# Kernel tuning notes

Measured on AMD Instinct MI355X. Metric: run time of the kernel, lower is better.

The kernel has to match this reference:

```python
import jax, jax.numpy as jnp
import numpy as np

E = 1024          # n_embed_dim
H = 64            # head_size = n_embed_dim // n_heads (16)

def setup_inputs() -> dict:
    key = jax.random.key(0)
    k_x, k_q, k_k, k_v = jax.random.split(key, 4)
    scale = 1.0 / np.sqrt(E)
    return {
        "x": jax.random.normal(k_x, (4, 2048, E), dtype=jnp.float32),
        "ln_gamma": jnp.ones((E,), jnp.float32),
        "ln_beta": jnp.zeros((E,), jnp.float32),
        # torch nn.Linear weights: [out_features, in_features]
        "Wq": jax.random.normal(k_q, (H, E), dtype=jnp.float32) * scale,
        "Wk": jax.random.normal(k_k, (H, E), dtype=jnp.float32) * scale,
        "Wv": jax.random.normal(k_v, (H, E), dtype=jnp.float32) * scale,
    }

def reference(x, ln_gamma, ln_beta, Wq, Wk, Wv):
    # LayerNorm over last dim (eps matches torch default 1e-5)
    mu = jnp.mean(x, axis=-1, keepdims=True)
    var = jnp.mean(jnp.square(x - mu), axis=-1, keepdims=True)
    xn = (x - mu) * jax.lax.rsqrt(var + 1e-5) * ln_gamma + ln_beta

    q = jnp.einsum('bse,he->bsh', xn, Wq)   # [B,S,H]
    k = jnp.einsum('bse,he->bsh', xn, Wk)
    v = jnp.einsum('bse,he->bsh', xn, Wv)

    scores = jnp.einsum('bqh,bkh->bqk', q, k) / jnp.sqrt(jnp.float32(H))
    S = x.shape[1]
    causal = jnp.tril(jnp.ones((S, S), dtype=bool))
    scores = jnp.where(causal, scores, -jnp.inf)
    attn = jax.nn.softmax(scores, axis=-1)
    return jnp.einsum('bqk,bkh->bqh', attn, v)
```

## Files before the change

kernel.cpp:

```cpp
#include <hip/hip_runtime.h>

#define E 1024
#define HH 64
#define BB 4
#define SS 2048
#define BS (BB*SS)
#define NSLOT 144

typedef unsigned short u16;
typedef short bf16x8 __attribute__((ext_vector_type(8)));
typedef float f32x4 __attribute__((ext_vector_type(4)));

#define LOG2E_O8 0.18033688011112042f

__device__ inline u16 f2bf(float f) {
    unsigned int u = __float_as_uint(f);
    unsigned int r = (u + 0x7FFFu + ((u >> 16) & 1u)) >> 16;
    return (u16)r;
}
__device__ inline float bf2f(u16 h) {
    return __uint_as_float(((unsigned int)h) << 16);
}

__global__ __launch_bounds__(256) void ln_wcast(const float* __restrict__ x,
        const float* __restrict__ gamma, const float* __restrict__ beta,
        const float* __restrict__ Wq, const float* __restrict__ Wk,
        const float* __restrict__ Wv,
        u16* __restrict__ xn, u16* __restrict__ wc) {
    const int t = threadIdx.x;
    if (blockIdx.x < 2048) {
        const int w = t >> 6, lane = t & 63;
        const size_t row = (size_t)blockIdx.x * 4 + w;
        const float4* xr = (const float4*)(x + row * E);
        float4 v[4];
        #pragma unroll
        for (int i = 0; i < 4; ++i) v[i] = xr[lane + 64 * i];
        float s = 0.f, sq = 0.f;
        #pragma unroll
        for (int i = 0; i < 4; ++i) {
            s  += v[i].x + v[i].y + v[i].z + v[i].w;
            sq += v[i].x*v[i].x + v[i].y*v[i].y + v[i].z*v[i].z + v[i].w*v[i].w;
        }
        #pragma unroll
        for (int off = 32; off > 0; off >>= 1) {
            s  += __shfl_xor(s,  off);
            sq += __shfl_xor(sq, off);
        }
        const float mean = s * (1.0f / E);
        const float var  = sq * (1.0f / E) - mean * mean;
        const float rstd = rsqrtf(var + 1e-5f);
        const float4* gr = (const float4*)gamma;
        const float4* br = (const float4*)beta;
        #pragma unroll
        for (int i = 0; i < 4; ++i) {
            const float4 g  = gr[lane + 64 * i];
            const float4 bt = br[lane + 64 * i];
            ushort4 o;
            o.x = f2bf((v[i].x - mean) * rstd * g.x + bt.x);
            o.y = f2bf((v[i].y - mean) * rstd * g.y + bt.y);
            o.z = f2bf((v[i].z - mean) * rstd * g.z + bt.z);
            o.w = f2bf((v[i].w - mean) * rstd * g.w + bt.w);
            *(ushort4*)(xn + row * E + (lane + 64 * i) * 4) = o;
        }
    } else {
        const int row = blockIdx.x - 2048;
        const float* src = (row < 64)  ? (Wq + (size_t)row * E)
                         : (row < 128) ? (Wk + (size_t)(row - 64) * E)
                                       : (Wv + (size_t)(row - 128) * E);
        const float sc = (row < 64) ? LOG2E_O8 : 1.0f;
        const float4 v = *(const float4*)(src + t * 4);
        ushort4 o;
        o.x = f2bf(v.x * sc); o.y = f2bf(v.y * sc);
        o.z = f2bf(v.z * sc); o.w = f2bf(v.w * sc);
        *(ushort4*)(wc + (size_t)row * E + t * 4) = o;
    }
}

__global__ __launch_bounds__(256) void qkv_mfma(const u16* __restrict__ xn,
        const u16* __restrict__ wc,
        u16* __restrict__ qb, u16* __restrict__ kb, u16* __restrict__ vt) {
    const int mb   = blockIdx.x >> 1;
    const int half = blockIdx.x & 1;
    const int row0 = mb * 32;
    const int t = threadIdx.x;
    const int w = t >> 6, lane = t & 63;
    const int quad = lane >> 4, r15 = lane & 15;
    const int mt = w >> 1, cgrp = w & 1;
    __shared__ u16 Xs[32 * 128];
    __shared__ u16 Ws[96 * 128];
    f32x4 acc[3] = {};
    const int xrow = mt * 16 + r15;

    for (int kc8 = 0; kc8 < 8; ++kc8) {
        __syncthreads();
        {
            const int row = t >> 3, ch = t & 7;
            #pragma unroll
            for (int hf = 0; hf < 2; ++hf) {
                const uint4 d = *(const uint4*)(xn + (size_t)(row0 + row) * E
                                                + kc8 * 128 + hf * 64 + ch * 8);
                *(uint4*)&Xs[row * 128 + hf * 64 + (ch ^ (row & 7)) * 8] = d;
            }
        }
        #pragma unroll
        for (int i = 0; i < 6; ++i) {
            const int idx = i * 256 + t;
            const int wl = idx >> 4, ch16 = idx & 15;
            const int hf = ch16 >> 3, ch = ch16 & 7;
            const uint4 d = *(const uint4*)(wc + (size_t)(half * 96 + wl) * E
                                            + kc8 * 128 + hf * 64 + ch * 8);
            *(uint4*)&Ws[wl * 128 + hf * 64 + (ch ^ (wl & 7)) * 8] = d;
        }
        __syncthreads();
        #pragma unroll
        for (int kk = 0; kk < 4; ++kk) {
            const int hf = kk >> 1, q4 = (kk & 1) * 4 + quad;
            const bf16x8 af = *(const bf16x8*)&Xs[xrow * 128 + hf * 64 + (q4 ^ (xrow & 7)) * 8];
            #pragma unroll
            for (int j = 0; j < 3; ++j) {
                const int wl = (cgrp * 3 + j) * 16 + r15;
                const bf16x8 bfr = *(const bf16x8*)&Ws[wl * 128 + hf * 64 + (q4 ^ (wl & 7)) * 8];
                acc[j] = __builtin_amdgcn_mfma_f32_16x16x32_bf16(af, bfr, acc[j], 0, 0, 0);
            }
        }
    }
    const int b    = row0 >> 11;
    const int key0 = row0 & 2047;
    #pragma unroll
    for (int j = 0; j < 3; ++j) {
        const int cg  = half * 96 + cgrp * 48 + j * 16 + r15;
        const int sel = cg >> 6;
        const int col = cg & 63;
        if (sel < 2) {
            u16* base = (sel == 0) ? qb : kb;
            #pragma unroll
            for (int r = 0; r < 4; ++r) {
                const size_t row = (size_t)row0 + mt * 16 + quad * 4 + r;
                base[row * HH + col] = f2bf(acc[j][r]);
            }
        } else {
            ushort4 pk;
            pk.x = f2bf(acc[j][0]); pk.y = f2bf(acc[j][1]);
            pk.z = f2bf(acc[j][2]); pk.w = f2bf(acc[j][3]);
            *(ushort4*)(vt + (size_t)b * HH * SS + (size_t)col * SS
                           + key0 + mt * 16 + quad * 4) = pk;
        }
    }
}

__global__ __launch_bounds__(256) void attn_partial(const u16* __restrict__ qb,
        const u16* __restrict__ kb, const u16* __restrict__ vt,
        u16* __restrict__ po, float* __restrict__ pl,
        float* __restrict__ out) {
    const int bid = blockIdx.x;
    const int b   = bid / 72;
    const int s2  = bid - b * 72;
    int a = (int)((sqrtf(4.0f * s2 + 1.0f) - 1.0f) * 0.5f);
    while ((a + 1) * (a + 2) <= s2) ++a;
    while (a * (a + 1) > s2) --a;
    const int rem = s2 - a * (a + 1);
    const int rp  = rem / (a + 1);
    const int c   = rem - rp * (a + 1);
    const int qt0 = 4 * a + 2 * rp;
    const int nc  = a + 1;
    const int t = threadIdx.x;
    const int w = t >> 6, lane = t & 63;
    const int quad = lane >> 4, r15 = lane & 15;

    __shared__ u16 Ks[4 * 64 * 64];
    __shared__ u16 VT[4 * 64 * 64];
    __shared__ u16 Ps[64 * 64];

    bf16x8 qf0[2], qf1[2];
    #pragma unroll
    for (int qi = 0; qi < 2; ++qi) {
        const size_t qrow = ((size_t)b * SS + (qt0 + qi) * 64 + w * 16 + r15) * HH;
        qf0[qi] = *(const bf16x8*)(qb + qrow + quad * 8);
        qf1[qi] = *(const bf16x8*)(qb + qrow + 32 + quad * 8);
    }

    const int ntmax = (c < a) ? 4 : (2 * rp + 2);

    {
        const int row = t >> 2, ch0 = (t & 3) * 2;
        for (int tl = 0; tl < ntmax; ++tl) {
            const int kt = (c * 4 + tl) << 6;
            const uint4* srcK = (const uint4*)(kb + ((size_t)b * SS + kt + row) * HH + ch0 * 8);
            const uint4 k0 = srcK[0], k1 = srcK[1];
            *(uint4*)&Ks[tl * 4096 + row * 64 + ((ch0    ) ^ (row & 7)) * 8] = k0;
            *(uint4*)&Ks[tl * 4096 + row * 64 + ((ch0 + 1) ^ (row & 7)) * 8] = k1;
            const uint4* srcV = (const uint4*)(vt + (size_t)b * HH * SS + (size_t)row * SS
                                               + kt + ch0 * 8);
            const uint4 v0 = srcV[0], v1 = srcV[1];
            *(uint4*)&VT[tl * 4096 + row * 64 + ((ch0    ) ^ (row & 7)) * 8] = v0;
            *(uint4*)&VT[tl * 4096 + row * 64 + ((ch0 + 1) ^ (row & 7)) * 8] = v1;
        }
    }
    __syncthreads();

    f32x4 o[2][4] = {};
    float l_[2][4] = {};

    for (int tl = 0; tl < ntmax; ++tl) {
        const int tile = c * 4 + tl;
        const u16* KsT = &Ks[tl * 4096];
        const u16* VTT = &VT[tl * 4096];

        bf16x8 kf0[4], kf1[4], vf0[4], vf1[4];
        #pragma unroll
        for (int nt = 0; nt < 4; ++nt) {
            const int krow = nt * 16 + r15;
            kf0[nt] = *(const bf16x8*)&KsT[krow * 64 + ((    quad) ^ (krow & 7)) * 8];
            kf1[nt] = *(const bf16x8*)&KsT[krow * 64 + ((4 + quad) ^ (krow & 7)) * 8];
            vf0[nt] = *(const bf16x8*)&VTT[krow * 64 + ((    quad) ^ (krow & 7)) * 8];
            vf1[nt] = *(const bf16x8*)&VTT[krow * 64 + ((4 + quad) ^ (krow & 7)) * 8];
        }

        #pragma unroll
        for (int qi = 0; qi < 2; ++qi) {
            const int qt_i = qt0 + qi;
            if (tile > qt_i) continue;

            f32x4 s4[4] = {};
            #pragma unroll
            for (int nt = 0; nt < 4; ++nt) {
                s4[nt] = __builtin_amdgcn_mfma_f32_16x16x32_bf16(qf0[qi], kf0[nt], s4[nt], 0, 0, 0);
                s4[nt] = __builtin_amdgcn_mfma_f32_16x16x32_bf16(qf1[qi], kf1[nt], s4[nt], 0, 0, 0);
            }
            if (tile == qt_i) {
                #pragma unroll
                for (int nt = 0; nt < 4; ++nt)
                    #pragma unroll
                    for (int r = 0; r < 4; ++r)
                        if (nt * 16 + r15 > w * 16 + quad * 4 + r) s4[nt][r] = -INFINITY;
            }

            float p[4][4];
            #pragma unroll
            for (int r = 0; r < 4; ++r) {
                #pragma unroll
                for (int nt = 0; nt < 4; ++nt)
                    p[nt][r] = __builtin_amdgcn_exp2f(s4[nt][r]);
                l_[qi][r] += (p[0][r] + p[1][r]) + (p[2][r] + p[3][r]);
            }

            #pragma unroll
            for (int nt = 0; nt < 4; ++nt)
                #pragma unroll
                for (int r = 0; r < 4; ++r) {
                    const int prow = w * 16 + quad * 4 + r;
                    const int col  = nt * 16 + r15;
                    Ps[prow * 64 + (((col >> 3) ^ (prow & 7)) * 8) + (col & 7)] = f2bf(p[nt][r]);
                }
            const int arow = w * 16 + r15;
            const bf16x8 pf0 = *(const bf16x8*)&Ps[arow * 64 + ((    quad) ^ (arow & 7)) * 8];
            const bf16x8 pf1 = *(const bf16x8*)&Ps[arow * 64 + ((4 + quad) ^ (arow & 7)) * 8];

            #pragma unroll
            for (int ht = 0; ht < 4; ++ht) {
                o[qi][ht] = __builtin_amdgcn_mfma_f32_16x16x32_bf16(pf0, vf0[ht], o[qi][ht], 0, 0, 0);
                o[qi][ht] = __builtin_amdgcn_mfma_f32_16x16x32_bf16(pf1, vf1[ht], o[qi][ht], 0, 0, 0);
            }
        }
    }

    #pragma unroll
    for (int qi = 0; qi < 2; ++qi)
        #pragma unroll
        for (int r = 0; r < 4; ++r) {
            l_[qi][r] += __shfl_xor(l_[qi][r], 1); l_[qi][r] += __shfl_xor(l_[qi][r], 2);
            l_[qi][r] += __shfl_xor(l_[qi][r], 4); l_[qi][r] += __shfl_xor(l_[qi][r], 8);
        }

    #pragma unroll
    for (int qi = 0; qi < 2; ++qi) {
        const int qt_i = qt0 + qi;
        if (nc == 1) {
            #pragma unroll
            for (int r = 0; r < 4; ++r) {
                const float inv = 1.0f / l_[qi][r];
                const size_t orow = ((size_t)b * SS + qt_i * 64 + w * 16 + quad * 4 + r) * HH;
                #pragma unroll
                for (int ht = 0; ht < 4; ++ht)
                    out[orow + ht * 16 + r15] = o[qi][ht][r] * inv;
            }
        } else {
            const int slot = b * NSLOT + 2 * a * (a + 1) + (2 * rp + qi) * (a + 1) + c;
            #pragma unroll
            for (int r = 0; r < 4; ++r) {
                const int q = w * 16 + quad * 4 + r;
                #pragma unroll
                for (int ht = 0; ht < 4; ++ht)
                    po[(size_t)slot * 4096 + q * 64 + ht * 16 + r15] = f2bf(o[qi][ht][r]);
                if (r15 == 0) pl[slot * 64 + q] = l_[qi][r];
            }
        }
    }
}

__global__ __launch_bounds__(256) void attn_reduce(const u16* __restrict__ po,
        const float* __restrict__ pl, float* __restrict__ out) {
    const int bid = blockIdx.x;
    const int b = bid / 112, rem = bid - b * 112;
    const int qt = 4 + (rem >> 2), qq = rem & 3;
    const int a = qt >> 2, r_ = qt & 3;
    const int nc = a + 1;
    const int sbase = b * NSLOT + 2 * a * (a + 1) + r_ * (a + 1);
    const int t = threadIdx.x;
    const int h = t & 63, qr = t >> 6;
    #pragma unroll
    for (int i = 0; i < 4; ++i) {
        const int q = qq * 16 + qr * 4 + i;
        float osum = 0.f, lsum = 0.f;
        for (int cidx = 0; cidx < nc; ++cidx) {
            osum += bf2f(po[(size_t)(sbase + cidx) * 4096 + q * 64 + h]);
            lsum += pl[(sbase + cidx) * 64 + q];
        }
        out[((size_t)b * SS + (qt << 6) + q) * HH + h] = osum / lsum;
    }
}

extern "C" void kernel_launch(void* const* d_in, const int* in_sizes, int n_in,
                              void* d_out, int out_size, void* d_ws, size_t ws_size,
                              hipStream_t stream) {
    const float* x     = (const float*)d_in[0];
    const float* gamma = (const float*)d_in[1];
    const float* beta  = (const float*)d_in[2];
    const float* Wq    = (const float*)d_in[3];
    const float* Wk    = (const float*)d_in[4];
    const float* Wv    = (const float*)d_in[5];
    float* out = (float*)d_out;

    char* p = (char*)d_ws;
    u16*   xn   = (u16*)p;                         p += (size_t)BS * E * 2;
    u16*   wc   = (u16*)p;                         p += 393216;
    u16*   qb   = (u16*)p;                         p += (size_t)BS * HH * 2;
    u16*   kb   = (u16*)p;                         p += (size_t)BS * HH * 2;
    u16*   vt   = (u16*)p;                         p += (size_t)BS * HH * 2;
    u16*   po   = (u16*)p;                         p += (size_t)BB * NSLOT * 4096 * 2;
    float* pl   = (float*)p;

    ln_wcast    <<<2048 + 192,  256, 0, stream>>>(x, gamma, beta, Wq, Wk, Wv, xn, wc);
    qkv_mfma    <<<BS / 16,     256, 0, stream>>>(xn, wc, qb, kb, vt);
    attn_partial<<<BB * 72,     256, 0, stream>>>(qb, kb, vt, po, pl, out);
    attn_reduce <<<BB * 112,    256, 0, stream>>>(po, pl, out);
}
```

Baseline: 118.8 us.

## Fuse attention split-K reduce into partial kernel via atomic last-block counter

Removes the separate attn_reduce launch. Each partial block now increments a per-(batch, query-tile-pair) atomic counter, and the last-arriving block sums the bf16 partial outputs and row sums and writes the final output. The counters are zeroed by an extra block in the layernorm kernel. This saves one kernel launch and its tail, but the final reduction is serialized onto a single block per group, and it adds threadfence and atomic overhead.

Result: slower. 200.4 us (+68.7%).

```diff
diff --git a/kernel.cpp b/kernel.cpp
--- a/kernel.cpp
+++ b/kernel.cpp
@@ -26,7 +26,7 @@
         const float* __restrict__ gamma, const float* __restrict__ beta,
         const float* __restrict__ Wq, const float* __restrict__ Wk,
         const float* __restrict__ Wv,
-        u16* __restrict__ xn, u16* __restrict__ wc) {
+        u16* __restrict__ xn, u16* __restrict__ wc, int* __restrict__ cnt) {
     const int t = threadIdx.x;
     if (blockIdx.x < 2048) {
         const int w = t >> 6, lane = t & 63;
@@ -62,6 +62,8 @@
             o.w = f2bf((v[i].w - mean) * rstd * g.w + bt.w);
             *(ushort4*)(xn + row * E + (lane + 64 * i) * 4) = o;
         }
+    } else if (blockIdx.x == 2240) {
+        if (t < 64) cnt[t] = 0;
     } else {
         const int row = blockIdx.x - 2048;
         const float* src = (row < 64)  ? (Wq + (size_t)row * E)
@@ -151,7 +153,7 @@
 __global__ __launch_bounds__(256) void attn_partial(const u16* __restrict__ qb,
         const u16* __restrict__ kb, const u16* __restrict__ vt,
         u16* __restrict__ po, float* __restrict__ pl,
-        float* __restrict__ out) {
+        int* __restrict__ cnt, float* __restrict__ out) {
     const int bid = blockIdx.x;
     const int b   = bid / 72;
     const int s2  = bid - b * 72;
@@ -272,10 +274,10 @@
             l_[qi][r] += __shfl_xor(l_[qi][r], 4); l_[qi][r] += __shfl_xor(l_[qi][r], 8);
         }
 
-    #pragma unroll
-    for (int qi = 0; qi < 2; ++qi) {
-        const int qt_i = qt0 + qi;
-        if (nc == 1) {
+    if (nc == 1) {
+        #pragma unroll
+        for (int qi = 0; qi < 2; ++qi) {
+            const int qt_i = qt0 + qi;
             #pragma unroll
             for (int r = 0; r < 4; ++r) {
                 const float inv = 1.0f / l_[qi][r];
@@ -284,39 +286,47 @@
                 for (int ht = 0; ht < 4; ++ht)
                     out[orow + ht * 16 + r15] = o[qi][ht][r] * inv;
             }
-        } else {
-            const int slot = b * NSLOT + 2 * a * (a + 1) + (2 * rp + qi) * (a + 1) + c;
-            #pragma unroll
-            for (int r = 0; r < 4; ++r) {
-                const int q = w * 16 + quad * 4 + r;
-                #pragma unroll
-                for (int ht = 0; ht < 4; ++ht)
-                    po[(size_t)slot * 4096 + q * 64 + ht * 16 + r15] = f2bf(o[qi][ht][r]);
-                if (r15 == 0) pl[slot * 64 + q] = l_[qi][r];
-            }
-        }
-    }
-}
-
-__global__ __launch_bounds__(256) void attn_reduce(const u16* __restrict__ po,
-        const float* __restrict__ pl, float* __restrict__ out) {
-    const int bid = blockIdx.x;
-    const int b = bid / 112, rem = bid - b * 112;
-    const int qt = 4 + (rem >> 2), qq = rem & 3;
-    const int a = qt >> 2, r_ = qt & 3;
-    const int nc = a + 1;
-    const int sbase = b * NSLOT + 2 * a * (a + 1) + r_ * (a + 1);
-    const int t = threadIdx.x;
-    const int h = t & 63, qr = t >> 6;
+        }
+        return;
+    }
+
     #pragma unroll
-    for (int i = 0; i < 4; ++i) {
-        const int q = qq * 16 + qr * 4 + i;
-        float osum = 0.f, lsum = 0.f;
-        for (int cidx = 0; cidx < nc; ++cidx) {
-            osum += bf2f(po[(size_t)(sbase + cidx) * 4096 + q * 64 + h]);
-            lsum += pl[(sbase + cidx) * 64 + q];
-        }
-        out[((size_t)b * SS + (qt << 6) + q) * HH + h] = osum / lsum;
+    for (int qi = 0; qi < 2; ++qi) {
+        const int slot = b * NSLOT + 2 * a * (a + 1) + (2 * rp + qi) * (a + 1) + c;
+        #pragma unroll
+        for (int r = 0; r < 4; ++r) {
+            const int q = w * 16 + quad * 4 + r;
+            #pragma unroll
+            for (int ht = 0; ht < 4; ++ht)
+                po[(size_t)slot * 4096 + q * 64 + ht * 16 + r15] = f2bf(o[qi][ht][r]);
+            if (r15 == 0) pl[slot * 64 + q] = l_[qi][r];
+        }
+    }
+
+    __shared__ int tick;
+    __syncthreads();
+    if (t == 0) {
+        __threadfence();
+        tick = atomicAdd(&cnt[b * 16 + a * 2 + rp], 1);
+    }
+    __syncthreads();
+    if (tick == nc - 1) {
+        __threadfence();
+        const int h = t & 63, qr = t >> 6;
+        #pragma unroll
+        for (int qi = 0; qi < 2; ++qi) {
+            const int qt_i = qt0 + qi;
+            const int sbase = b * NSLOT + 2 * a * (a + 1) + (2 * rp + qi) * (a + 1);
+            for (int i = 0; i < 16; ++i) {
+                const int q = qr * 16 + i;
+                float osum = 0.f, lsum = 0.f;
+                for (int cidx = 0; cidx < nc; ++cidx) {
+                    osum += bf2f(po[(size_t)(sbase + cidx) * 4096 + q * 64 + h]);
+                    lsum += pl[(sbase + cidx) * 64 + q];
+                }
+                out[((size_t)b * SS + (qt_i << 6) + q) * HH + h] = osum / lsum;
+            }
+        }
     }
 }
 
@@ -338,10 +348,10 @@
     u16*   kb   = (u16*)p;                         p += (size_t)BS * HH * 2;
     u16*   vt   = (u16*)p;                         p += (size_t)BS * HH * 2;
     u16*   po   = (u16*)p;                         p += (size_t)BB * NSLOT * 4096 * 2;
-    float* pl   = (float*)p;
-
-    ln_wcast    <<<2048 + 192,  256, 0, stream>>>(x, gamma, beta, Wq, Wk, Wv, xn, wc);
-    qkv_mfma    <<<BS / 16,     256, 0, stream>>>(xn, wc, qb, kb, vt);
-    attn_partial<<<BB * 72,     256, 0, stream>>>(qb, kb, vt, po, pl, out);
-    attn_reduce <<<BB * 112,    256, 0, stream>>>(po, pl, out);
-}
+    float* pl   = (float*)p;                       p += (size_t)BB * NSLOT * 64 * 4;
+    int*   cnt  = (int*)p;
+
+    ln_wcast    <<<2048 + 192 + 1, 256, 0, stream>>>(x, gamma, beta, Wq, Wk, Wv, xn, wc, cnt);
+    qkv_mfma    <<<BS / 16,        256, 0, stream>>>(xn, wc, qb, kb, vt);
+    attn_partial<<<BB * 72,        256, 0, stream>>>(qb, kb, vt, po, pl, cnt, out);
+}
```

## Fuse LayerNorm and weight cast into QKV projection kernel with double-buffered weights

Applied to the files above, without the earlier changes.

Merges the LayerNorm/bf16-cast kernel into the QKV MFMA kernel. Each block normalizes its 32 rows directly into shared memory (all 8 K-chunks resident), and casts fp32 weights to bf16 on the fly into a double-buffered LDS tile. This removes the global round trip of the bf16 normalized activations and one launch. The cost is that each pair of blocks recomputes LayerNorm for the same rows, weights are re-read and re-cast per block, and LDS use grows enough to limit occupancy to one block. The Q scale moves to the epilogue, and the reduce loop is unrolled with a predicate.

Result: slower. 133.7 us (+12.6%).

```diff
diff --git a/kernel.cpp b/kernel.cpp
--- a/kernel.cpp
+++ b/kernel.cpp
@@ -21,63 +21,14 @@
 __device__ inline float bf2f(u16 h) {
     return __uint_as_float(((unsigned int)h) << 16);
 }
-
-__global__ __launch_bounds__(256) void ln_wcast(const float* __restrict__ x,
+__device__ inline unsigned int pk2(float lo, float hi) {
+    return (unsigned int)f2bf(lo) | ((unsigned int)f2bf(hi) << 16);
+}
+
+__global__ __launch_bounds__(256, 1) void lnqkv(const float* __restrict__ x,
         const float* __restrict__ gamma, const float* __restrict__ beta,
         const float* __restrict__ Wq, const float* __restrict__ Wk,
         const float* __restrict__ Wv,
-        u16* __restrict__ xn, u16* __restrict__ wc) {
-    const int t = threadIdx.x;
-    if (blockIdx.x < 2048) {
-        const int w = t >> 6, lane = t & 63;
-        const size_t row = (size_t)blockIdx.x * 4 + w;
-        const float4* xr = (const float4*)(x + row * E);
-        float4 v[4];
-        #pragma unroll
-        for (int i = 0; i < 4; ++i) v[i] = xr[lane + 64 * i];
-        float s = 0.f, sq = 0.f;
-        #pragma unroll
-        for (int i = 0; i < 4; ++i) {
-            s  += v[i].x + v[i].y + v[i].z + v[i].w;
-            sq += v[i].x*v[i].x + v[i].y*v[i].y + v[i].z*v[i].z + v[i].w*v[i].w;
-        }
-        #pragma unroll
-        for (int off = 32; off > 0; off >>= 1) {
-            s  += __shfl_xor(s,  off);
-            sq += __shfl_xor(sq, off);
-        }
-        const float mean = s * (1.0f / E);
-        const float var  = sq * (1.0f / E) - mean * mean;
-        const float rstd = rsqrtf(var + 1e-5f);
-        const float4* gr = (const float4*)gamma;
-        const float4* br = (const float4*)beta;
-        #pragma unroll
-        for (int i = 0; i < 4; ++i) {
-            const float4 g  = gr[lane + 64 * i];
-            const float4 bt = br[lane + 64 * i];
-            ushort4 o;
-            o.x = f2bf((v[i].x - mean) * rstd * g.x + bt.x);
-            o.y = f2bf((v[i].y - mean) * rstd * g.y + bt.y);
-            o.z = f2bf((v[i].z - mean) * rstd * g.z + bt.z);
-            o.w = f2bf((v[i].w - mean) * rstd * g.w + bt.w);
-            *(ushort4*)(xn + row * E + (lane + 64 * i) * 4) = o;
-        }
-    } else {
-        const int row = blockIdx.x - 2048;
-        const float* src = (row < 64)  ? (Wq + (size_t)row * E)
-                         : (row < 128) ? (Wk + (size_t)(row - 64) * E)
-                                       : (Wv + (size_t)(row - 128) * E);
-        const float sc = (row < 64) ? LOG2E_O8 : 1.0f;
-        const float4 v = *(const float4*)(src + t * 4);
-        ushort4 o;
-        o.x = f2bf(v.x * sc); o.y = f2bf(v.y * sc);
-        o.z = f2bf(v.z * sc); o.w = f2bf(v.w * sc);
-        *(ushort4*)(wc + (size_t)row * E + t * 4) = o;
-    }
-}
-
-__global__ __launch_bounds__(256) void qkv_mfma(const u16* __restrict__ xn,
-        const u16* __restrict__ wc,
         u16* __restrict__ qb, u16* __restrict__ kb, u16* __restrict__ vt) {
     const int mb   = blockIdx.x >> 1;
     const int half = blockIdx.x & 1;
@@ -86,44 +37,101 @@
     const int w = t >> 6, lane = t & 63;
     const int quad = lane >> 4, r15 = lane & 15;
     const int mt = w >> 1, cgrp = w & 1;
-    __shared__ u16 Xs[32 * 128];
-    __shared__ u16 Ws[96 * 128];
+    __shared__ u16 Xs[8 * 32 * 128];
+    __shared__ u16 Ws[2][96 * 128];
     f32x4 acc[3] = {};
     const int xrow = mt * 16 + r15;
 
-    for (int kc8 = 0; kc8 < 8; ++kc8) {
-        __syncthreads();
-        {
-            const int row = t >> 3, ch = t & 7;
-            #pragma unroll
-            for (int hf = 0; hf < 2; ++hf) {
-                const uint4 d = *(const uint4*)(xn + (size_t)(row0 + row) * E
-                                                + kc8 * 128 + hf * 64 + ch * 8);
-                *(uint4*)&Xs[row * 128 + hf * 64 + (ch ^ (row & 7)) * 8] = d;
-            }
-        }
+    {
+        const float4* gr = (const float4*)gamma;
+        const float4* br = (const float4*)beta;
+        float4 g[4], bt[4];
+        #pragma unroll
+        for (int i = 0; i < 4; ++i) { g[i] = gr[lane + 64 * i]; bt[i] = br[lane + 64 * i]; }
+        #pragma unroll
+        for (int rb = 0; rb < 2; ++rb) {
+            float4 v[4][4];
+            #pragma unroll
+            for (int rr = 0; rr < 4; ++rr) {
+                const int row = w * 8 + rb * 4 + rr;
+                const float4* xr = (const float4*)(x + (size_t)(row0 + row) * E);
+                #pragma unroll
+                for (int i = 0; i < 4; ++i) v[rr][i] = xr[lane + 64 * i];
+            }
+            #pragma unroll
+            for (int rr = 0; rr < 4; ++rr) {
+                const int row = w * 8 + rb * 4 + rr;
+                float s = 0.f, sq = 0.f;
+                #pragma unroll
+                for (int i = 0; i < 4; ++i) {
+                    s  += v[rr][i].x + v[rr][i].y + v[rr][i].z + v[rr][i].w;
+                    sq += v[rr][i].x*v[rr][i].x + v[rr][i].y*v[rr][i].y
+                        + v[rr][i].z*v[rr][i].z + v[rr][i].w*v[rr][i].w;
+                }
+                #pragma unroll
+                for (int off = 32; off > 0; off >>= 1) {
+                    s  += __shfl_xor(s,  off);
+                    sq += __shfl_xor(sq, off);
+                }
+                const float mean = s * (1.0f / E);
+                const float var  = sq * (1.0f / E) - mean * mean;
+                const float rstd = rsqrtf(var + 1e-5f);
+                #pragma unroll
+                for (int i = 0; i < 4; ++i) {
+                    ushort4 o;
+                    o.x = f2bf((v[rr][i].x - mean) * rstd * g[i].x + bt[i].x);
+                    o.y = f2bf((v[rr][i].y - mean) * rstd * g[i].y + bt[i].y);
+                    o.z = f2bf((v[rr][i].z - mean) * rstd * g[i].z + bt[i].z);
+                    o.w = f2bf((v[rr][i].w - mean) * rstd * g[i].w + bt[i].w);
+                    const int p = lane + 64 * i;
+                    const int dst = (p >> 5) * 4096 + row * 128 + ((p >> 4) & 1) * 64
+                                  + ((((p >> 1) & 7) ^ (row & 7)) * 8) + (p & 1) * 4;
+                    *(ushort4*)&Xs[dst] = o;
+                }
+            }
+        }
+    }
+
+    auto stageW = [&](int kc, int buf) {
         #pragma unroll
         for (int i = 0; i < 6; ++i) {
             const int idx = i * 256 + t;
-            const int wl = idx >> 4, ch16 = idx & 15;
-            const int hf = ch16 >> 3, ch = ch16 & 7;
-            const uint4 d = *(const uint4*)(wc + (size_t)(half * 96 + wl) * E
-                                            + kc8 * 128 + hf * 64 + ch * 8);
-            *(uint4*)&Ws[wl * 128 + hf * 64 + (ch ^ (wl & 7)) * 8] = d;
-        }
-        __syncthreads();
+            const int wl = idx >> 4, u = idx & 15;
+            const int hf = u >> 3, ch = u & 7;
+            const int grow = half * 96 + wl;
+            const float* src = (grow < 64)  ? (Wq + (size_t)grow * E)
+                             : (grow < 128) ? (Wk + (size_t)(grow - 64) * E)
+                                            : (Wv + (size_t)(grow - 128) * E);
+            const float4 a  = *(const float4*)(src + kc * 128 + u * 8);
+            const float4 b2 = *(const float4*)(src + kc * 128 + u * 8 + 4);
+            uint4 d;
+            d.x = pk2(a.x,  a.y);  d.y = pk2(a.z,  a.w);
+            d.z = pk2(b2.x, b2.y); d.w = pk2(b2.z, b2.w);
+            *(uint4*)&Ws[buf][wl * 128 + hf * 64 + (ch ^ (wl & 7)) * 8] = d;
+        }
+    };
+
+    stageW(0, 0);
+    __syncthreads();
+
+    for (int kc8 = 0; kc8 < 8; ++kc8) {
+        const int cur = kc8 & 1;
+        if (kc8 < 7) stageW(kc8 + 1, cur ^ 1);
+        const u16* Xc = &Xs[kc8 * 4096];
         #pragma unroll
         for (int kk = 0; kk < 4; ++kk) {
             const int hf = kk >> 1, q4 = (kk & 1) * 4 + quad;
-            const bf16x8 af = *(const bf16x8*)&Xs[xrow * 128 + hf * 64 + (q4 ^ (xrow & 7)) * 8];
+            const bf16x8 af = *(const bf16x8*)&Xc[xrow * 128 + hf * 64 + (q4 ^ (xrow & 7)) * 8];
             #pragma unroll
             for (int j = 0; j < 3; ++j) {
                 const int wl = (cgrp * 3 + j) * 16 + r15;
-                const bf16x8 bfr = *(const bf16x8*)&Ws[wl * 128 + hf * 64 + (q4 ^ (wl & 7)) * 8];
+                const bf16x8 bfr = *(const bf16x8*)&Ws[cur][wl * 128 + hf * 64 + (q4 ^ (wl & 7)) * 8];
                 acc[j] = __builtin_amdgcn_mfma_f32_16x16x32_bf16(af, bfr, acc[j], 0, 0, 0);
             }
         }
-    }
+        __syncthreads();
+    }
+
     const int b    = row0 >> 11;
     const int key0 = row0 & 2047;
     #pragma unroll
@@ -133,10 +141,11 @@
         const int col = cg & 63;
         if (sel < 2) {
             u16* base = (sel == 0) ? qb : kb;
+            const float esc = (sel == 0) ? LOG2E_O8 : 1.0f;
             #pragma unroll
             for (int r = 0; r < 4; ++r) {
                 const size_t row = (size_t)row0 + mt * 16 + quad * 4 + r;
-                base[row * HH + col] = f2bf(acc[j][r]);
+                base[row * HH + col] = f2bf(acc[j][r] * esc);
             }
         } else {
             ushort4 pk;
@@ -312,9 +321,12 @@
     for (int i = 0; i < 4; ++i) {
         const int q = qq * 16 + qr * 4 + i;
         float osum = 0.f, lsum = 0.f;
-        for (int cidx = 0; cidx < nc; ++cidx) {
-            osum += bf2f(po[(size_t)(sbase + cidx) * 4096 + q * 64 + h]);
-            lsum += pl[(sbase + cidx) * 64 + q];
+        #pragma unroll
+        for (int cidx = 0; cidx < 8; ++cidx) {
+            if (cidx < nc) {
+                osum += bf2f(po[(size_t)(sbase + cidx) * 4096 + q * 64 + h]);
+                lsum += pl[(sbase + cidx) * 64 + q];
+            }
         }
         out[((size_t)b * SS + (qt << 6) + q) * HH + h] = osum / lsum;
     }
@@ -332,16 +344,13 @@
     float* out = (float*)d_out;
 
     char* p = (char*)d_ws;
-    u16*   xn   = (u16*)p;                         p += (size_t)BS * E * 2;
-    u16*   wc   = (u16*)p;                         p += 393216;
     u16*   qb   = (u16*)p;                         p += (size_t)BS * HH * 2;
     u16*   kb   = (u16*)p;                         p += (size_t)BS * HH * 2;
     u16*   vt   = (u16*)p;                         p += (size_t)BS * HH * 2;
     u16*   po   = (u16*)p;                         p += (size_t)BB * NSLOT * 4096 * 2;
     float* pl   = (float*)p;
 
-    ln_wcast    <<<2048 + 192,  256, 0, stream>>>(x, gamma, beta, Wq, Wk, Wv, xn, wc);
-    qkv_mfma    <<<BS / 16,     256, 0, stream>>>(xn, wc, qb, kb, vt);
-    attn_partial<<<BB * 72,     256, 0, stream>>>(qb, kb, vt, po, pl, out);
-    attn_reduce <<<BB * 112,    256, 0, stream>>>(po, pl, out);
-}
+    lnqkv       <<<BS / 16,  256, 0, stream>>>(x, gamma, beta, Wq, Wk, Wv, qb, kb, vt);
+    attn_partial<<<BB * 72,  256, 0, stream>>>(qb, kb, vt, po, pl, out);
+    attn_reduce <<<BB * 112, 256, 0, stream>>>(po, pl, out);
+}
```

## Pre-swizzle QKV operands and double-buffer LDS with direct global-to-LDS loads

Applied to the files above, without the earlier changes.

The LayerNorm/cast kernel now writes xn and the cast weights in a pre-swizzled order, so the QKV GEMM can copy tiles straight into LDS with global_load_lds. It no longer passes them through registers. The GEMM double-buffers its LDS tiles and issues the next k-chunk's loads before computing the current one, overlapping memory with MFMA work. The reduce kernel's chunk loop is unrolled to a fixed bound of 8 with a guard. This costs twice the LDS, and correctness depends on the stored swizzle exactly matching the LDS layout the MFMA reads expect.

New measurement: 119.3 us. Within noise of the previous version (+0.4%).

```diff
diff --git a/kernel.cpp b/kernel.cpp
--- a/kernel.cpp
+++ b/kernel.cpp
@@ -20,6 +20,12 @@
 }
 __device__ inline float bf2f(u16 h) {
     return __uint_as_float(((unsigned int)h) << 16);
+}
+__device__ inline void gl2lds(const u16* g, u16* l) {
+    __builtin_amdgcn_global_load_lds(
+        (const __attribute__((address_space(1))) unsigned int*)g,
+        (__attribute__((address_space(3))) unsigned int*)l,
+        16, 0, 0);
 }
 
 __global__ __launch_bounds__(256) void ln_wcast(const float* __restrict__ x,
@@ -31,6 +37,7 @@
     if (blockIdx.x < 2048) {
         const int w = t >> 6, lane = t & 63;
         const size_t row = (size_t)blockIdx.x * 4 + w;
+        const int r7 = (int)(row & 7);
         const float4* xr = (const float4*)(x + row * E);
         float4 v[4];
         #pragma unroll
@@ -60,7 +67,10 @@
             o.y = f2bf((v[i].y - mean) * rstd * g.y + bt.y);
             o.z = f2bf((v[i].z - mean) * rstd * g.z + bt.z);
             o.w = f2bf((v[i].w - mean) * rstd * g.w + bt.w);
-            *(ushort4*)(xn + row * E + (lane + 64 * i) * 4) = o;
+            const int p = lane + 64 * i;
+            const int dst = (p >> 5) * 128 + ((p >> 4) & 1) * 64
+                          + ((((p >> 1) & 7) ^ r7) * 8) + (p & 1) * 4;
+            *(ushort4*)(xn + row * E + dst) = o;
         }
     } else {
         const int row = blockIdx.x - 2048;
@@ -72,7 +82,9 @@
         ushort4 o;
         o.x = f2bf(v.x * sc); o.y = f2bf(v.y * sc);
         o.z = f2bf(v.z * sc); o.w = f2bf(v.w * sc);
-        *(ushort4*)(wc + (size_t)row * E + t * 4) = o;
+        const int dst = (t >> 5) * 128 + ((t >> 4) & 1) * 64
+                      + ((((t >> 1) & 7) ^ (row & 7)) * 8) + (t & 1) * 4;
+        *(ushort4*)(wc + (size_t)row * E + dst) = o;
     }
 }
 
@@ -86,44 +98,46 @@
     const int w = t >> 6, lane = t & 63;
     const int quad = lane >> 4, r15 = lane & 15;
     const int mt = w >> 1, cgrp = w & 1;
-    __shared__ u16 Xs[32 * 128];
-    __shared__ u16 Ws[96 * 128];
+    __shared__ u16 Xs[2][32 * 128];
+    __shared__ u16 Ws[2][96 * 128];
     f32x4 acc[3] = {};
     const int xrow = mt * 16 + r15;
 
+    const int srow = t >> 4, u = t & 15;
+
+    auto stage = [&](int kc, int buf) {
+        gl2lds(xn + (size_t)(row0 + srow) * E + kc * 128 + u * 8,
+               &Xs[buf][w * 512]);
+        gl2lds(xn + (size_t)(row0 + 16 + srow) * E + kc * 128 + u * 8,
+               &Xs[buf][2048 + w * 512]);
+        #pragma unroll
+        for (int i = 0; i < 6; ++i) {
+            const int wl = i * 16 + srow;
+            gl2lds(wc + (size_t)(half * 96 + wl) * E + kc * 128 + u * 8,
+                   &Ws[buf][i * 2048 + w * 512]);
+        }
+    };
+
+    stage(0, 0);
+    __syncthreads();
+
     for (int kc8 = 0; kc8 < 8; ++kc8) {
-        __syncthreads();
-        {
-            const int row = t >> 3, ch = t & 7;
-            #pragma unroll
-            for (int hf = 0; hf < 2; ++hf) {
-                const uint4 d = *(const uint4*)(xn + (size_t)(row0 + row) * E
-                                                + kc8 * 128 + hf * 64 + ch * 8);
-                *(uint4*)&Xs[row * 128 + hf * 64 + (ch ^ (row & 7)) * 8] = d;
-            }
-        }
-        #pragma unroll
-        for (int i = 0; i < 6; ++i) {
-            const int idx = i * 256 + t;
-            const int wl = idx >> 4, ch16 = idx & 15;
-            const int hf = ch16 >> 3, ch = ch16 & 7;
-            const uint4 d = *(const uint4*)(wc + (size_t)(half * 96 + wl) * E
-                                            + kc8 * 128 + hf * 64 + ch * 8);
-            *(uint4*)&Ws[wl * 128 + hf * 64 + (ch ^ (wl & 7)) * 8] = d;
-        }
-        __syncthreads();
+        const int cur = kc8 & 1;
+        if (kc8 < 7) stage(kc8 + 1, cur ^ 1);
         #pragma unroll
         for (int kk = 0; kk < 4; ++kk) {
             const int hf = kk >> 1, q4 = (kk & 1) * 4 + quad;
-            const bf16x8 af = *(const bf16x8*)&Xs[xrow * 128 + hf * 64 + (q4 ^ (xrow & 7)) * 8];
+            const bf16x8 af = *(const bf16x8*)&Xs[cur][xrow * 128 + hf * 64 + (q4 ^ (xrow & 7)) * 8];
             #pragma unroll
             for (int j = 0; j < 3; ++j) {
                 const int wl = (cgrp * 3 + j) * 16 + r15;
-                const bf16x8 bfr = *(const bf16x8*)&Ws[wl * 128 + hf * 64 + (q4 ^ (wl & 7)) * 8];
+                const bf16x8 bfr = *(const bf16x8*)&Ws[cur][wl * 128 + hf * 64 + (q4 ^ (wl & 7)) * 8];
                 acc[j] = __builtin_amdgcn_mfma_f32_16x16x32_bf16(af, bfr, acc[j], 0, 0, 0);
             }
         }
-    }
+        __syncthreads();
+    }
+
     const int b    = row0 >> 11;
     const int key0 = row0 & 2047;
     #pragma unroll
@@ -312,9 +326,12 @@
     for (int i = 0; i < 4; ++i) {
         const int q = qq * 16 + qr * 4 + i;
         float osum = 0.f, lsum = 0.f;
-        for (int cidx = 0; cidx < nc; ++cidx) {
-            osum += bf2f(po[(size_t)(sbase + cidx) * 4096 + q * 64 + h]);
-            lsum += pl[(sbase + cidx) * 64 + q];
+        #pragma unroll
+        for (int cidx = 0; cidx < 8; ++cidx) {
+            if (cidx < nc) {
+                osum += bf2f(po[(size_t)(sbase + cidx) * 4096 + q * 64 + h]);
+                lsum += pl[(sbase + cidx) * 64 + q];
+            }
         }
         out[((size_t)b * SS + (qt << 6) + q) * HH + h] = osum / lsum;
     }
```
